# Optimization experiments

Hardware: AMD Instinct MI355X
Metric: run time of the kernel (lower is better)

Reference implementation:

```python
import jax, jax.numpy as jnp
import numpy as np

B, H, W = 16, 1024, 1024
EPS = 1e-7
FG_PROB = 0.1  # foreground pixel probability for synthetic gt


def setup_inputs() -> dict:
    key = jax.random.key(0)
    k1, k2 = jax.random.split(key)
    probs = jax.random.normal(k1, (B, 2, H, W), dtype=jnp.float32)
    gt = (jax.random.uniform(k2, (B, H, W)) < FG_PROB).astype(jnp.float32)
    gt_f_num = gt.sum(axis=(1, 2))  # per-sample foreground pixel count (float)
    return {"probs": probs, "gt": gt, "gt_f_num": gt_f_num, "img_h": H, "img_w": W}


def reference(probs, gt, gt_f_num, img_h, img_w):
    # foreground probability, clamped
    pc = jax.nn.softmax(probs, axis=1)[:, 1, :, :]
    pc = jnp.clip(pc, EPS, 1.0 - EPS)
    b = pc.shape[0]
    f_loss = -(gt * jnp.log(pc)).reshape(b, -1)          # [B, N]
    b_loss = -((1.0 - gt) * jnp.log(1.0 - pc)).reshape(b, -1)  # [B, N]
    n = b_loss.shape[1]

    # sort background loss descending per sample; top gt_f_num[i] entries are
    # "difficult" negatives, the rest are "simple" (equivalent to the torch
    # gather-into-zero-buffers since only sums/counts are taken afterwards)
    sorted_b = -jnp.sort(-b_loss, axis=1)                # descending, [B, N]
    k = gt_f_num.astype(jnp.int32)                       # int(gt_f_num[i])
    mask = jnp.arange(n, dtype=jnp.int32)[None, :] < k[:, None]  # [B, N]

    difficult_sum = jnp.sum(jnp.where(mask, sorted_b, 0.0), axis=1)
    simple_sum = jnp.sum(jnp.where(mask, 0.0, sorted_b), axis=1)
    difficult_num = jnp.sum(mask & (sorted_b != 0.0), axis=1).astype(jnp.float32)

    difficult_b_loss = difficult_sum / (difficult_num + 1e-16)
    simple_b_loss = simple_sum / (float(img_h * img_w) + 1e-16)
    f_loss_mean = f_loss.sum(axis=1) / (gt_f_num + 1e-16)

    return difficult_b_loss.mean() + f_loss_mean.mean() + simple_b_loss.mean()
```

## Files before the change

### kernel.cpp

```cpp
#include <hip/hip_runtime.h>
#include <math.h>

#define NB 16
#define NPIX 1048576
#define BINS 4096
#define HBINS (BINS / 2)
#define DUMMY_W HBINS
#define CHUNKS 64
#define TPB_A 256
#define PIX_PER_BLOCK (NPIX / CHUNKS)
#define PPT 4
#define ITERS_A (PIX_PER_BLOCK / (TPB_A * PPT))
#define TPB_B 256
#define BINS_PER_CHUNK (BINS / TPB_B)
#define WORDS_PER_THREAD (HBINS / TPB_B)
#define BLOSS_MAX 16.2f
#define BINW (BLOSS_MAX / (float)BINS)
#define B_CAP 15.9424f
#define F_CAP 16.1181f

typedef float f32x4 __attribute__((ext_vector_type(4)));

__global__ __launch_bounds__(TPB_A, 8) void pass_a(
    const float* __restrict__ probs, const float* __restrict__ gt,
    unsigned* __restrict__ g_hist, float* __restrict__ f_part,
    float* __restrict__ b_part)
{
    __shared__ unsigned s_cnt[HBINS + 8];
    __shared__ float s_redf[TPB_A / 64];
    __shared__ float s_redb[TPB_A / 64];

    const int tid = threadIdx.x;
    for (int j = tid; j < HBINS + 8; j += TPB_A) s_cnt[j] = 0u;
    __syncthreads();

    const int blk = blockIdx.x;
    const int b = blk / CHUNKS;
    const int chunk = blk % CHUNKS;
    const float* p0 = probs + (size_t)b * 2 * NPIX;
    const float* p1 = p0 + NPIX;
    const float* gp = gt + (size_t)b * NPIX;
    const int base = chunk * PIX_PER_BLOCK;
    const float scale = (float)BINS / BLOSS_MAX;

    float f_acc = 0.f, b_acc = 0.f;

    for (int it = 0; it < ITERS_A; ++it) {
        const int i = base + it * (TPB_A * PPT) + (tid << 2);
        const f32x4 a = __builtin_nontemporal_load((const f32x4*)(p0 + i));
        const f32x4 c = __builtin_nontemporal_load((const f32x4*)(p1 + i));
        const f32x4 g = __builtin_nontemporal_load((const f32x4*)(gp + i));
        const float dv[PPT] = {c.x - a.x, c.y - a.y, c.z - a.z, c.w - a.w};
        const float gv[PPT] = {g.x, g.y, g.z, g.w};
        #pragma unroll
        for (int q = 0; q < PPT; ++q) {
            const float d = dv[q];
            const float sp = fmaxf(d, 0.f) + __logf(1.f + __expf(-fabsf(d)));
            const bool fg = gv[q] > 0.5f;
            const float fl = fminf(sp - d, F_CAP);
            const float bl = fminf(sp, B_CAP);
            f_acc += fg ? fl : 0.f;
            b_acc += fg ? 0.f : bl;
            int bin = (int)(bl * scale);
            bin = bin < (BINS - 1) ? bin : (BINS - 1);
            const int word = fg ? DUMMY_W : (bin >> 1);
            const unsigned inc = 1u << ((bin & 1) << 4);
            atomicAdd(&s_cnt[word], inc);
        }
    }
    __syncthreads();

    unsigned* dst = g_hist + ((size_t)b * CHUNKS + chunk) * HBINS;
    for (int j = tid; j < HBINS; j += TPB_A) dst[j] = s_cnt[j];

    #pragma unroll
    for (int o = 32; o > 0; o >>= 1) {
        f_acc += __shfl_down(f_acc, o, 64);
        b_acc += __shfl_down(b_acc, o, 64);
    }
    if ((tid & 63) == 0) { s_redf[tid >> 6] = f_acc; s_redb[tid >> 6] = b_acc; }
    __syncthreads();
    if (tid == 0) {
        float f = 0.f, bs = 0.f;
        #pragma unroll
        for (int w = 0; w < TPB_A / 64; ++w) { f += s_redf[w]; bs += s_redb[w]; }
        f_part[b * CHUNKS + chunk] = f;
        b_part[b * CHUNKS + chunk] = bs;
    }
}

__global__ __launch_bounds__(TPB_B) void pass_b(
    const unsigned* __restrict__ g_hist, const float* __restrict__ f_part,
    const float* __restrict__ b_part, const float* __restrict__ gt_f_num,
    float* __restrict__ terms)
{
    __shared__ unsigned s_suf[TPB_B];
    __shared__ double s_wsuf[TPB_B];
    __shared__ double s_dsum;
    __shared__ double s_fb[2];

    const int b = blockIdx.x;
    const int t = threadIdx.x;

    unsigned cnt[BINS_PER_CHUNK];
    #pragma unroll
    for (int j = 0; j < BINS_PER_CHUNK; ++j) cnt[j] = 0u;
    const unsigned* hb = g_hist + (size_t)b * CHUNKS * HBINS + t * WORDS_PER_THREAD;
    #pragma unroll 4
    for (int c = 0; c < CHUNKS; ++c) {
        const uint4 w0 = *(const uint4*)(hb + (size_t)c * HBINS);
        const uint4 w1 = *(const uint4*)(hb + (size_t)c * HBINS + 4);
        cnt[0]  += w0.x & 0xFFFFu;  cnt[1]  += w0.x >> 16;
        cnt[2]  += w0.y & 0xFFFFu;  cnt[3]  += w0.y >> 16;
        cnt[4]  += w0.z & 0xFFFFu;  cnt[5]  += w0.z >> 16;
        cnt[6]  += w0.w & 0xFFFFu;  cnt[7]  += w0.w >> 16;
        cnt[8]  += w1.x & 0xFFFFu;  cnt[9]  += w1.x >> 16;
        cnt[10] += w1.y & 0xFFFFu;  cnt[11] += w1.y >> 16;
        cnt[12] += w1.z & 0xFFFFu;  cnt[13] += w1.z >> 16;
        cnt[14] += w1.w & 0xFFFFu;  cnt[15] += w1.w >> 16;
    }

    const int cb = t * BINS_PER_CHUNK;
    unsigned c = 0; double w = 0.0;
    #pragma unroll
    for (int j = 0; j < BINS_PER_CHUNK; ++j) {
        c += cnt[j];
        w += (double)cnt[j] * (double)(((float)(cb + j) + 0.5f) * BINW);
    }
    s_suf[t] = c; s_wsuf[t] = w;

    if (t < 64) {
        double ff = (double)f_part[b * CHUNKS + t];
        double bb = (double)b_part[b * CHUNKS + t];
        #pragma unroll
        for (int o = 32; o > 0; o >>= 1) {
            ff += __shfl_down(ff, o, 64);
            bb += __shfl_down(bb, o, 64);
        }
        if (t == 0) { s_fb[0] = ff; s_fb[1] = bb; }
    }
    __syncthreads();

    for (int off = 1; off < TPB_B; off <<= 1) {
        const unsigned ac = (t + off < TPB_B) ? s_suf[t + off] : 0u;
        const double aw = (t + off < TPB_B) ? s_wsuf[t + off] : 0.0;
        __syncthreads();
        s_suf[t] += ac; s_wsuf[t] += aw;
        __syncthreads();
    }

    const long long kk = (long long)gt_f_num[b];
    const unsigned long long n_pos = (unsigned long long)s_suf[0];
    const unsigned long long suf_me = s_suf[t];
    const unsigned long long suf_nx = (t + 1 < TPB_B) ? s_suf[t + 1] : 0ull;

    if (kk > 0 && (unsigned long long)kk < n_pos &&
        suf_nx < (unsigned long long)kk && (unsigned long long)kk <= suf_me) {
        unsigned long long cum = suf_nx;
        double W = (t + 1 < TPB_B) ? s_wsuf[t + 1] : 0.0;
        int bstar = cb;
        for (int j = BINS_PER_CHUNK - 1; j >= 0; --j) {
            const unsigned cc = cnt[j];
            if (cum + cc >= (unsigned long long)kk) { bstar = cb + j; break; }
            cum += cc;
            W += (double)cc * (double)(((float)(cb + j) + 0.5f) * BINW);
        }
        const double partial = (double)(kk - (long long)cum);
        s_dsum = W + partial * (double)(((float)bstar + 0.5f) * BINW);
    }
    __syncthreads();

    if (t == 0) {
        const double S_total = s_fb[1];
        const double fs = s_fb[0];
        const double gfn = (double)gt_f_num[b];
        double dsum, dnum;
        if (kk <= 0) { dsum = 0.0; dnum = 0.0; }
        else if ((unsigned long long)kk >= n_pos) { dsum = S_total; dnum = (double)n_pos; }
        else { dsum = s_dsum; dnum = (double)kk; }
        const double term = dsum / (dnum + 1e-16)
                          + fs / (gfn + 1e-16)
                          + (S_total - dsum) / ((double)NPIX + 1e-16);
        terms[b] = (float)term;
    }
}

__global__ void pass_c(const float* __restrict__ terms, float* __restrict__ out)
{
    if (threadIdx.x == 0 && blockIdx.x == 0) {
        float s = 0.f;
        #pragma unroll
        for (int i = 0; i < NB; ++i) s += terms[i];
        out[0] = s / (float)NB;
    }
}

extern "C" void kernel_launch(void* const* d_in, const int* in_sizes, int n_in,
                              void* d_out, int out_size, void* d_ws, size_t ws_size,
                              hipStream_t stream) {
    const float* probs = (const float*)d_in[0];
    const float* gt    = (const float*)d_in[1];
    const float* gfn   = (const float*)d_in[2];
    char* ws = (char*)d_ws;

    const size_t hist_bytes = (size_t)NB * CHUNKS * HBINS * sizeof(unsigned);
    unsigned* g_hist = (unsigned*)ws;
    float*    f_part = (float*)(ws + hist_bytes);
    float*    b_part = f_part + NB * CHUNKS;
    float*    terms  = b_part + NB * CHUNKS;

    hipLaunchKernelGGL(pass_a, dim3(NB * CHUNKS), dim3(TPB_A), 0, stream,
                       probs, gt, g_hist, f_part, b_part);
    hipLaunchKernelGGL(pass_b, dim3(NB), dim3(TPB_B), 0, stream,
                       g_hist, f_part, b_part, gfn, terms);
    hipLaunchKernelGGL(pass_c, dim3(1), dim3(64), 0, stream,
                       terms, (float*)d_out);
}
```

Baseline: 234.0 us.

## Double-buffer pass_a input loads via async global-to-LDS prefetch

```diff
diff --git a/kernel.cpp b/kernel.cpp
--- a/kernel.cpp
+++ b/kernel.cpp
@@ -20,17 +20,28 @@
 #define F_CAP 16.1181f
 
 typedef float f32x4 __attribute__((ext_vector_type(4)));
-
-__global__ __launch_bounds__(TPB_A, 8) void pass_a(
+typedef unsigned u32x4 __attribute__((ext_vector_type(4)));
+
+#define GLB_AS __attribute__((address_space(1)))
+#define LDS_AS __attribute__((address_space(3)))
+
+__device__ __forceinline__ void gload16(const float* g, float* lds_wave_base) {
+    __builtin_amdgcn_global_load_lds((const GLB_AS void*)g,
+                                     (LDS_AS void*)lds_wave_base, 16, 0, 0);
+}
+
+__global__ __launch_bounds__(TPB_A, 4) void pass_a(
     const float* __restrict__ probs, const float* __restrict__ gt,
     unsigned* __restrict__ g_hist, float* __restrict__ f_part,
     float* __restrict__ b_part)
 {
     __shared__ unsigned s_cnt[HBINS + 8];
+    __shared__ __align__(16) float s_stage[2][3][TPB_A * PPT];
     __shared__ float s_redf[TPB_A / 64];
     __shared__ float s_redb[TPB_A / 64];
 
     const int tid = threadIdx.x;
+    const int wid = tid >> 6;
     for (int j = tid; j < HBINS + 8; j += TPB_A) s_cnt[j] = 0u;
     __syncthreads();
 
@@ -45,11 +56,36 @@
 
     float f_acc = 0.f, b_acc = 0.f;
 
+    {
+        const int i = base + (tid << 2);
+        float* wbase0 = &s_stage[0][0][wid * 256];
+        float* wbase1 = &s_stage[0][1][wid * 256];
+        float* wbase2 = &s_stage[0][2][wid * 256];
+        gload16(p0 + i, wbase0);
+        gload16(p1 + i, wbase1);
+        gload16(gp + i, wbase2);
+    }
+
     for (int it = 0; it < ITERS_A; ++it) {
-        const int i = base + it * (TPB_A * PPT) + (tid << 2);
-        const f32x4 a = __builtin_nontemporal_load((const f32x4*)(p0 + i));
-        const f32x4 c = __builtin_nontemporal_load((const f32x4*)(p1 + i));
-        const f32x4 g = __builtin_nontemporal_load((const f32x4*)(gp + i));
+        const int buf = it & 1;
+        if (it + 1 < ITERS_A) {
+            const int i = base + (it + 1) * (TPB_A * PPT) + (tid << 2);
+            float* wbase0 = &s_stage[buf ^ 1][0][wid * 256];
+            float* wbase1 = &s_stage[buf ^ 1][1][wid * 256];
+            float* wbase2 = &s_stage[buf ^ 1][2][wid * 256];
+            gload16(p0 + i, wbase0);
+            gload16(p1 + i, wbase1);
+            gload16(gp + i, wbase2);
+            asm volatile("s_waitcnt vmcnt(3)" ::: "memory");
+        } else {
+            asm volatile("s_waitcnt vmcnt(0)" ::: "memory");
+        }
+        __builtin_amdgcn_sched_barrier(0);
+
+        const int lo = tid << 2;
+        const f32x4 a = *(const f32x4*)&s_stage[buf][0][lo];
+        const f32x4 c = *(const f32x4*)&s_stage[buf][1][lo];
+        const f32x4 g = *(const f32x4*)&s_stage[buf][2][lo];
         const float dv[PPT] = {c.x - a.x, c.y - a.y, c.z - a.z, c.w - a.w};
         const float gv[PPT] = {g.x, g.y, g.z, g.w};
         #pragma unroll
@@ -108,8 +144,8 @@
     const unsigned* hb = g_hist + (size_t)b * CHUNKS * HBINS + t * WORDS_PER_THREAD;
     #pragma unroll 4
     for (int c = 0; c < CHUNKS; ++c) {
-        const uint4 w0 = *(const uint4*)(hb + (size_t)c * HBINS);
-        const uint4 w1 = *(const uint4*)(hb + (size_t)c * HBINS + 4);
+        const u32x4 w0 = __builtin_nontemporal_load((const u32x4*)(hb + (size_t)c * HBINS));
+        const u32x4 w1 = __builtin_nontemporal_load((const u32x4*)(hb + (size_t)c * HBINS + 4));
         cnt[0]  += w0.x & 0xFFFFu;  cnt[1]  += w0.x >> 16;
         cnt[2]  += w0.y & 0xFFFFu;  cnt[3]  += w0.y >> 16;
         cnt[4]  += w0.z & 0xFFFFu;  cnt[5]  += w0.z >> 16;
```

After: 254.9 us. 1.09x slower.
